# Performance work log

Measured on AMD Instinct MI355X. Metric: run time of the kernel, lower is better.

The kernel has to match this reference:

```python
import jax, jax.numpy as jnp
import numpy as np

NEG_SLOPE = 0.2


def gat_conv(x, src, dst, n, W, a_src, a_dst, b):
    # x: [N, Din], W: [Din, Dout], a_src/a_dst: [Dout], b: [Dout]
    h = x @ W                                   # [N, Dout]
    alpha_src = h @ a_src                       # [N] score contribution of source nodes
    alpha_dst = h @ a_dst                       # [N]
    e = jax.nn.leaky_relu(alpha_src[src] + alpha_dst[dst], NEG_SLOPE)  # [E]
    # segment softmax over destination nodes (every node has a self-loop -> no empty segs)
    m = jax.ops.segment_max(e, dst, num_segments=n)
    p = jnp.exp(e - m[dst])
    denom = jax.ops.segment_sum(p, dst, num_segments=n)
    coeff = p / denom[dst]                      # [E]
    out = jax.ops.segment_sum(h[src] * coeff[:, None], dst, num_segments=n)
    return out + b


def setup_inputs() -> dict:
    key = jax.random.key(0)
    ks = jax.random.split(key, 16)
    N, E, D_IN, D_H, C = 50000, 800000, 256, 256, 10
    x = jax.random.normal(ks[0], (N, D_IN), dtype=jnp.float32)
    edge_index = jax.random.randint(ks[1], (2, E), 0, N, dtype=jnp.int64)
    s = 0.1
    params = {
        "W1": jax.random.normal(ks[2], (D_IN, D_H), jnp.float32) * s,
        "a_src1": jax.random.normal(ks[3], (D_H,), jnp.float32) * s,
        "a_dst1": jax.random.normal(ks[4], (D_H,), jnp.float32) * s,
        "b1": jnp.zeros((D_H,), jnp.float32),
        "W2": jax.random.normal(ks[5], (D_H, D_H), jnp.float32) * s,
        "a_src2": jax.random.normal(ks[6], (D_H,), jnp.float32) * s,
        "a_dst2": jax.random.normal(ks[7], (D_H,), jnp.float32) * s,
        "b2": jnp.zeros((D_H,), jnp.float32),
        "W3": jax.random.normal(ks[8], (D_H, C), jnp.float32) * s,
        "a_src3": jax.random.normal(ks[9], (C,), jnp.float32) * s,
        "a_dst3": jax.random.normal(ks[10], (C,), jnp.float32) * s,
        "b3": jnp.zeros((C,), jnp.float32),
    }
    return {"x": x, "edge_index": edge_index, **params}


def reference(x, edge_index, W1, a_src1, a_dst1, b1, W2, a_src2, a_dst2, b2,
              W3, a_src3, a_dst3, b3):
    n = x.shape[0]
    # PyG GATConv default add_self_loops=True
    loops = jnp.arange(n, dtype=edge_index.dtype)
    src = jnp.concatenate([edge_index[0], loops])
    dst = jnp.concatenate([edge_index[1], loops])
    h = gat_conv(x, src, dst, n, W1, a_src1, a_dst1, b1)
    h = jax.nn.relu(h)
    h = gat_conv(h, src, dst, n, W2, a_src2, a_dst2, b2)
    h = jax.nn.relu(h)
    out = gat_conv(h, src, dst, n, W3, a_src3, a_dst3, b3)
    return out
```

## Files before the change

kernel.cpp:

```cpp
#include <hip/hip_runtime.h>
#include <math.h>

#define N_NODES 50000
#define N_EDGES 800000
#define EP (N_EDGES + N_NODES)
#define NEG_SLOPE 0.2f
#define SCAN_BLOCKS ((N_NODES + 255) / 256)
#define COUNT_BLOCKS ((EP + 255) / 256)

typedef short short8 __attribute__((ext_vector_type(8)));
typedef float float4_ __attribute__((ext_vector_type(4)));

__device__ __forceinline__ unsigned short f2bf(float f) {
  unsigned int u = __float_as_uint(f);
  u = (u + 0x7FFFu + ((u >> 16) & 1u)) >> 16;
  return (unsigned short)u;
}
__device__ __forceinline__ float bf2f(unsigned int us) {
  return __uint_as_float(us << 16);
}
__device__ __forceinline__ unsigned int pack2(float lo, float hi) {
  return (unsigned int)f2bf(lo) | ((unsigned int)f2bf(hi) << 16);
}

__device__ __forceinline__ int permc(int p) {
  return ((p & 0xE) << 4) | ((p & 1) << 4) | (p >> 4);
}


__global__ void setup_kernel(const float* __restrict__ W1, const float* __restrict__ W2,
                             const float* __restrict__ W3, const float* __restrict__ b1,
                             const float* __restrict__ b2, const int* __restrict__ ei,
                             unsigned short* __restrict__ Wf1, unsigned short* __restrict__ Wf2,
                             unsigned short* __restrict__ Wf3,
                             float* __restrict__ pb1, float* __restrict__ pb2,
                             int* __restrict__ cnt) {
  int blk = blockIdx.x;
  int tid = threadIdx.x;
  if (blk >= 67) {
    int e = (blk - 67) * 256 + tid;
    if (e < EP) {
      int dst = (e < N_EDGES) ? ei[N_EDGES + e] : (e - N_EDGES);
      atomicAdd(&cnt[dst], 1);
    }
    return;
  }
  if (blk < 64) {
    int perm = blk >= 32;
    const float* W = perm ? W2 : W1;
    unsigned short* Wf = perm ? Wf2 : Wf1;
    int t = (blk & 31) * 256 + tid;
    int f = t >> 6, lane = t & 63;
    int nt = f >> 3, k0t = f & 7;
    int lm = lane & 15, kg = lane >> 4;
    int kbase = k0t * 32 + kg * 8;
    int n = nt * 16 + lm;
    short8 v;
#pragma unroll
    for (int j = 0; j < 8; ++j) {
      int k = perm ? permc(kbase + j) : (kbase + j);
      v[j] = (short)f2bf(W[(size_t)k * 256 + n]);
    }
    ((short8*)Wf)[t] = v;
  } else if (blk < 66) {
    int t = (blk - 64) * 256 + tid;
    int k0t = t >> 6, lane = t & 63;
    int lm = lane & 15, kg = lane >> 4;
    int kbase = k0t * 32 + kg * 8;
    short8 v;
#pragma unroll
    for (int j = 0; j < 8; ++j) {
      int k = permc(kbase + j);
      v[j] = (lm < 10) ? (short)f2bf(W3[(size_t)k * 10 + lm]) : (short)0;
    }
    ((short8*)Wf3)[t] = v;
  } else {
    int c = permc(tid);
    pb1[tid] = b1[c];
    pb2[tid] = b2[c];
  }
}


__global__ void scan12_kernel(const int* __restrict__ cnt, int* __restrict__ off,
                              int* __restrict__ bsum, int* __restrict__ bpre,
                              int* __restrict__ done) {
  int i = blockIdx.x * 256 + threadIdx.x;
  int v = (i < N_NODES) ? cnt[i] : 0;
  int lane = threadIdx.x & 63, w = threadIdx.x >> 6;
  int x = v;
  for (int o = 1; o < 64; o <<= 1) { int y = __shfl_up(x, o); if (lane >= o) x += y; }
  __shared__ int wsum[4];
  if (lane == 63) wsum[w] = x;
  __syncthreads();
  int add = 0;
  for (int k = 0; k < w; ++k) add += wsum[k];
  if (i < N_NODES) off[i] = x - v + add;
  __shared__ int amLast;
  if (threadIdx.x == 255) {
    bsum[blockIdx.x] = add + x;
    __threadfence();
    amLast = (atomicAdd(done, 1) == SCAN_BLOCKS - 1);
  }
  __syncthreads();
  if (amLast) {
    int t = threadIdx.x;
    int v2 = (t < SCAN_BLOCKS) ? atomicAdd(&bsum[t], 0) : 0;
    int x2 = v2;
    for (int o = 1; o < 64; o <<= 1) { int y = __shfl_up(x2, o); if (lane >= o) x2 += y; }
    __shared__ int wsum2[4];
    if (lane == 63) wsum2[w] = x2;
    __syncthreads();
    int add2 = 0;
    for (int k = 0; k < w; ++k) add2 += wsum2[k];
    if (t < SCAN_BLOCKS) bpre[t] = x2 - v2 + add2;
    if (t == SCAN_BLOCKS - 1) off[N_NODES] = v2;
  }
}

__global__ void scatter_kernel(const int* __restrict__ ei, const int* __restrict__ off,
                               const int* __restrict__ bpre, int* __restrict__ cnt,
                               int* __restrict__ esrc) {
  int e = blockIdx.x * 256 + threadIdx.x;
  if (e >= EP) return;
  int src, dst;
  if (e < N_EDGES) { src = ei[e]; dst = ei[N_EDGES + e]; }
  else { src = dst = e - N_EDGES; }
  int pos = off[dst] + bpre[dst >> 8] + atomicSub(&cnt[dst], 1) - 1;
  esrc[pos] = src;
}


template <int AF32>
__global__ __launch_bounds__(896, 1) void gemm_mfma5(const void* __restrict__ Av,
                                                     const uint4* __restrict__ Wf,
                                                     unsigned short* __restrict__ C,
                                                     const float* __restrict__ asrc,
                                                     const float* __restrict__ adst,
                                                     float* __restrict__ as_,
                                                     float* __restrict__ ad_, int M) {
  __shared__ uint4 Bl[8192];
  int tid = threadIdx.x;
  for (int i = tid; i < 8192; i += 896) Bl[i] = Wf[i];
  int wave = tid >> 6, lane = tid & 63;
  int lm = lane & 15, kg = lane >> 4;
  int row0 = blockIdx.x * 224 + wave * 16;
  int ar = row0 + lm;
  if (ar >= M) ar = M - 1;
  float4_ acc[16];
#pragma unroll
  for (int i = 0; i < 16; ++i) acc[i] = (float4_){0, 0, 0, 0};
  __syncthreads();
  const short8* Bf = (const short8*)Bl;
  for (int k0t = 0; k0t < 8; ++k0t) {
    int k0 = k0t * 32;
    short8 a;
    if (AF32) {
      const float* A = (const float*)Av;
      const float* p = A + (size_t)ar * 256 + kg * 8 + k0;
      float4 f0 = *(const float4*)p, f1 = *(const float4*)(p + 4);
      a = (short8){(short)f2bf(f0.x), (short)f2bf(f0.y), (short)f2bf(f0.z), (short)f2bf(f0.w),
                   (short)f2bf(f1.x), (short)f2bf(f1.y), (short)f2bf(f1.z), (short)f2bf(f1.w)};
    } else {
      const unsigned short* A = (const unsigned short*)Av;
      a = *(const short8*)(A + (size_t)ar * 256 + kg * 8 + k0);
    }
#pragma unroll
    for (int nt = 0; nt < 16; ++nt) {
      short8 b = Bf[(nt * 8 + k0t) * 64 + lane];
      acc[nt] = __builtin_amdgcn_mfma_f32_16x16x32_bf16(a, b, acc[nt], 0, 0, 0);
    }
  }
  float avs[16], avd[16];
#pragma unroll
  for (int nt = 0; nt < 16; ++nt) { avs[nt] = asrc[nt * 16 + lm]; avd[nt] = adst[nt * 16 + lm]; }
#pragma unroll
  for (int i = 0; i < 4; ++i) {
    int r = row0 + kg * 4 + i;
    float s = 0.f, dd = 0.f;
    unsigned int u[8];
#pragma unroll
    for (int j = 0; j < 8; ++j) {
      float vlo = acc[2 * j][i];
      float vhi = acc[2 * j + 1][i];
      u[j] = pack2(vlo, vhi);
      s += vlo * avs[2 * j] + vhi * avs[2 * j + 1];
      dd += vlo * avd[2 * j] + vhi * avd[2 * j + 1];
    }
    if (r < M) {
      uint4* cp = (uint4*)(C + (size_t)r * 256 + lm * 16);
      cp[0] = (uint4){u[0], u[1], u[2], u[3]};
      cp[1] = (uint4){u[4], u[5], u[6], u[7]};
    }
#pragma unroll
    for (int o = 1; o < 16; o <<= 1) { s += __shfl_xor(s, o); dd += __shfl_xor(dd, o); }
    if (lm == 0 && r < M) { as_[r] = s; ad_[r] = dd; }
  }
}


__global__ __launch_bounds__(448) void gemm_c3_kernel(const unsigned short* __restrict__ X,
                                                      const unsigned short* __restrict__ Wf3,
                                                      const float* __restrict__ asrc,
                                                      const float* __restrict__ adst,
                                                      float* __restrict__ h3,
                                                      float* __restrict__ as_,
                                                      float* __restrict__ ad_, int M) {
  int tid = threadIdx.x;
  int wave = tid >> 6, lane = tid & 63;
  int lm = lane & 15, kg = lane >> 4;
  int row0 = blockIdx.x * 224 + wave * 32;
  int ar0 = row0 + lm, ar1 = row0 + 16 + lm;
  if (ar0 >= M) ar0 = M - 1;
  if (ar1 >= M) ar1 = M - 1;
  short8 bf[8];
#pragma unroll
  for (int k0t = 0; k0t < 8; ++k0t) bf[k0t] = ((const short8*)Wf3)[k0t * 64 + lane];
  float4_ acc0 = (float4_){0, 0, 0, 0}, acc1 = (float4_){0, 0, 0, 0};
#pragma unroll
  for (int k0t = 0; k0t < 8; ++k0t) {
    int k0 = k0t * 32;
    short8 a0 = *(const short8*)(X + (size_t)ar0 * 256 + kg * 8 + k0);
    short8 a1 = *(const short8*)(X + (size_t)ar1 * 256 + kg * 8 + k0);
    acc0 = __builtin_amdgcn_mfma_f32_16x16x32_bf16(a0, bf[k0t], acc0, 0, 0, 0);
    acc1 = __builtin_amdgcn_mfma_f32_16x16x32_bf16(a1, bf[k0t], acc1, 0, 0, 0);
  }
  float avs = (lm < 10) ? asrc[lm] : 0.f;
  float avd = (lm < 10) ? adst[lm] : 0.f;
#pragma unroll
  for (int g = 0; g < 2; ++g) {
    int rbase = row0 + g * 16 + kg * 4;
#pragma unroll
    for (int i = 0; i < 4; ++i) {
      int r = rbase + i;
      float v = g ? acc1[i] : acc0[i];
      if (r < M && lm < 10) h3[(size_t)r * 10 + lm] = v;
      float s = v * avs, dd = v * avd;
#pragma unroll
      for (int o = 1; o < 16; o <<= 1) { s += __shfl_xor(s, o); dd += __shfl_xor(dd, o); }
      if (lm == 0 && r < M) { as_[r] = s; ad_[r] = dd; }
    }
  }
}


__global__ __launch_bounds__(256) void agg_fused_kernel(const int* __restrict__ off,
                                                        const int* __restrict__ bpre,
                                                        const int* __restrict__ esrc,
                                                        const float* __restrict__ as_,
                                                        const float* __restrict__ ad_,
                                                        const unsigned short* __restrict__ h,
                                                        const float* __restrict__ pbias,
                                                        unsigned short* __restrict__ outg) {
  __shared__ int s_src[4][64];
  __shared__ float s_p[4][64];
  int wave = threadIdx.x >> 6, lane = threadIdx.x & 63;
  int pair = lane >> 5, cl = lane & 31;
  int d = blockIdx.x * 4 + wave;
  int s0 = off[d] + bpre[d >> 8];
  int s1 = off[d + 1] + bpre[(d + 1) >> 8];
  float adv = ad_[d];
  const uint4* hp4 = (const uint4*)h;
  float a0 = 0.f, a1 = 0.f, a2 = 0.f, a3 = 0.f, a4 = 0.f, a5 = 0.f, a6 = 0.f, a7 = 0.f;
  float sum = 0.f;
  for (int base = s0; base < s1; base += 64) {
    int m = s1 - base; if (m > 64) m = 64;
    int sv = 0; float p = 0.f;
    if (lane < m) {
      sv = esrc[base + lane];
      float e = as_[sv] + adv;
      e = e > 0.f ? e : NEG_SLOPE * e;
      p = __expf(e);
    }
    s_src[wave][lane] = sv;
    s_p[wave][lane] = p;
    float ps = p;
    for (int o = 32; o; o >>= 1) ps += __shfl_xor(ps, o);
    sum += ps;
    int nb = (m + 1) >> 1;
    int j = 0;
    for (; j + 4 <= nb; j += 4) {
#pragma unroll
      for (int u = 0; u < 4; ++u) {
        int idx = (j + u) * 2 + pair;
        int src = s_src[wave][idx];
        float w = s_p[wave][idx];
        uint4 pv = hp4[(size_t)src * 32 + cl];
        a0 = fmaf(w, bf2f(pv.x & 0xffffu), a0); a1 = fmaf(w, bf2f(pv.x >> 16), a1);
        a2 = fmaf(w, bf2f(pv.y & 0xffffu), a2); a3 = fmaf(w, bf2f(pv.y >> 16), a3);
        a4 = fmaf(w, bf2f(pv.z & 0xffffu), a4); a5 = fmaf(w, bf2f(pv.z >> 16), a5);
        a6 = fmaf(w, bf2f(pv.w & 0xffffu), a6); a7 = fmaf(w, bf2f(pv.w >> 16), a7);
      }
    }
    for (; j < nb; ++j) {
      int idx = j * 2 + pair;
      int src = s_src[wave][idx];
      float w = s_p[wave][idx];
      uint4 pv = hp4[(size_t)src * 32 + cl];
      a0 = fmaf(w, bf2f(pv.x & 0xffffu), a0); a1 = fmaf(w, bf2f(pv.x >> 16), a1);
      a2 = fmaf(w, bf2f(pv.y & 0xffffu), a2); a3 = fmaf(w, bf2f(pv.y >> 16), a3);
      a4 = fmaf(w, bf2f(pv.z & 0xffffu), a4); a5 = fmaf(w, bf2f(pv.z >> 16), a5);
      a6 = fmaf(w, bf2f(pv.w & 0xffffu), a6); a7 = fmaf(w, bf2f(pv.w >> 16), a7);
    }
  }
  a0 += __shfl_xor(a0, 32); a1 += __shfl_xor(a1, 32);
  a2 += __shfl_xor(a2, 32); a3 += __shfl_xor(a3, 32);
  a4 += __shfl_xor(a4, 32); a5 += __shfl_xor(a5, 32);
  a6 += __shfl_xor(a6, 32); a7 += __shfl_xor(a7, 32);
  if (pair == 0) {
    float inv = 1.0f / sum;
    float4 b0 = ((const float4*)pbias)[2 * cl];
    float4 b1 = ((const float4*)pbias)[2 * cl + 1];
    float o0 = fmaxf(fmaf(a0, inv, b0.x), 0.f);
    float o1 = fmaxf(fmaf(a1, inv, b0.y), 0.f);
    float o2 = fmaxf(fmaf(a2, inv, b0.z), 0.f);
    float o3 = fmaxf(fmaf(a3, inv, b0.w), 0.f);
    float o4 = fmaxf(fmaf(a4, inv, b1.x), 0.f);
    float o5 = fmaxf(fmaf(a5, inv, b1.y), 0.f);
    float o6 = fmaxf(fmaf(a6, inv, b1.z), 0.f);
    float o7 = fmaxf(fmaf(a7, inv, b1.w), 0.f);
    uint4 ov = (uint4){pack2(o0, o1), pack2(o2, o3), pack2(o4, o5), pack2(o6, o7)};
    ((uint4*)outg)[(size_t)d * 32 + cl] = ov;
  }
}


__global__ void agg10_fused_kernel(const int* __restrict__ off, const int* __restrict__ bpre,
                                   const int* __restrict__ esrc,
                                   const float* __restrict__ as_, const float* __restrict__ ad_,
                                   const float* __restrict__ h, const float* __restrict__ bias,
                                   float* __restrict__ out) {
  int gid = blockIdx.x * 256 + threadIdx.x;
  int wid = gid >> 6, lane = threadIdx.x & 63;
  int g = lane >> 4, c = lane & 15;
  int d = wid * 4 + g;
  if (d >= N_NODES) return;
  int s0 = off[d] + bpre[d >> 8];
  int s1 = off[d + 1] + bpre[(d + 1) >> 8];
  float adv = ad_[d];
  float acc = 0.f, sum = 0.f;
  int s = s0;
  for (; s + 2 <= s1; s += 2) {
    int i0 = esrc[s], i1 = esrc[s + 1];
    float e0 = as_[i0] + adv; e0 = e0 > 0.f ? e0 : NEG_SLOPE * e0;
    float e1 = as_[i1] + adv; e1 = e1 > 0.f ? e1 : NEG_SLOPE * e1;
    float h0 = (c < 10) ? h[(size_t)i0 * 10 + c] : 0.f;
    float h1 = (c < 10) ? h[(size_t)i1 * 10 + c] : 0.f;
    float p0 = __expf(e0), p1 = __expf(e1);
    acc = fmaf(p0, h0, acc);
    acc = fmaf(p1, h1, acc);
    sum += p0 + p1;
  }
  if (s < s1) {
    int i0 = esrc[s];
    float e0 = as_[i0] + adv; e0 = e0 > 0.f ? e0 : NEG_SLOPE * e0;
    float p0 = __expf(e0);
    if (c < 10) acc = fmaf(p0, h[(size_t)i0 * 10 + c], acc);
    sum += p0;
  }
  if (c < 10) out[(size_t)d * 10 + c] = fmaf(acc, 1.0f / sum, bias[c]);
}


extern "C" void kernel_launch(void* const* d_in, const int* in_sizes, int n_in,
                              void* d_out, int out_size, void* d_ws, size_t ws_size,
                              hipStream_t stream) {
  const float* x   = (const float*)d_in[0];
  const int*   ei  = (const int*)d_in[1];
  const float* W1  = (const float*)d_in[2];
  const float* as1 = (const float*)d_in[3];
  const float* ad1 = (const float*)d_in[4];
  const float* b1  = (const float*)d_in[5];
  const float* W2  = (const float*)d_in[6];
  const float* as2 = (const float*)d_in[7];
  const float* ad2 = (const float*)d_in[8];
  const float* b2  = (const float*)d_in[9];
  const float* W3  = (const float*)d_in[10];
  const float* as3 = (const float*)d_in[11];
  const float* ad3 = (const float*)d_in[12];
  const float* b3  = (const float*)d_in[13];
  float* out = (float*)d_out;

  char* ws = (char*)d_ws;
  size_t off_b = 0;
  auto alloc = [&](size_t bytes) -> char* {
    char* p = ws + off_b;
    off_b += (bytes + 255) & ~(size_t)255;
    return p;
  };
  unsigned short* hb   = (unsigned short*)alloc((size_t)N_NODES * 256 * 2);
  unsigned short* gb   = (unsigned short*)alloc((size_t)N_NODES * 256 * 2);
  unsigned short* Wf1  = (unsigned short*)alloc(256 * 256 * 2);
  unsigned short* Wf2  = (unsigned short*)alloc(256 * 256 * 2);
  unsigned short* Wf3  = (unsigned short*)alloc(8 * 64 * 8 * 2);
  float* pb1   = (float*)alloc(256 * 4);
  float* pb2   = (float*)alloc(256 * 4);
  float* h3    = (float*)alloc((size_t)N_NODES * 10 * 4);
  float* as_   = (float*)alloc((size_t)N_NODES * 4);
  float* ad_   = (float*)alloc((size_t)N_NODES * 4);
  int*   roff  = (int*)alloc((size_t)(N_NODES + 1) * 4);
  int*   cnt   = (int*)alloc((size_t)(N_NODES + 64) * 4);
  int*   done  = cnt + N_NODES;
  int*   bsum  = (int*)alloc((size_t)SCAN_BLOCKS * 4);
  int*   bpre  = (int*)alloc((size_t)SCAN_BLOCKS * 4);
  int*   esrc  = (int*)alloc((size_t)EP * 4);

  hipMemsetAsync(cnt, 0, (size_t)(N_NODES + 1) * 4, stream);
  setup_kernel<<<67 + COUNT_BLOCKS, 256, 0, stream>>>(W1, W2, W3, b1, b2, ei,
                                                      Wf1, Wf2, Wf3, pb1, pb2, cnt);
  scan12_kernel<<<SCAN_BLOCKS, 256, 0, stream>>>(cnt, roff, bsum, bpre, done);
  scatter_kernel<<<COUNT_BLOCKS, 256, 0, stream>>>(ei, roff, bpre, cnt, esrc);

  int gblocks = (N_NODES + 223) / 224;
  int ablocks = (N_NODES + 3) / 4;

  gemm_mfma5<1><<<gblocks, 896, 0, stream>>>(x, (const uint4*)Wf1, hb, as1, ad1, as_, ad_, N_NODES);
  agg_fused_kernel<<<ablocks, 256, 0, stream>>>(roff, bpre, esrc, as_, ad_, hb, pb1, gb);
  gemm_mfma5<0><<<gblocks, 896, 0, stream>>>(gb, (const uint4*)Wf2, hb, as2, ad2, as_, ad_, N_NODES);
  agg_fused_kernel<<<ablocks, 256, 0, stream>>>(roff, bpre, esrc, as_, ad_, hb, pb2, gb);
  gemm_c3_kernel<<<gblocks, 448, 0, stream>>>(gb, Wf3, as3, ad3, h3, as_, ad_, N_NODES);
  agg10_fused_kernel<<<ablocks, 256, 0, stream>>>(roff, bpre, esrc, as_, ad_, h3, b3, out);
}
```

Before: 371.5 us.

## Fuse layer-3 projection into layer-2 aggregation epilogue and widen GEMM blocks

Removes the separate layer-3 GEMM kernel by computing the 10-wide projection and the folded attention scores (W3·a_src3, W3·a_dst3 precomputed in setup) in the epilogue of the second aggregation, using fp32 weights held in shared memory and a 32-lane shuffle reduction. This avoids rereading the 50000x256 bf16 activation buffer and saves a kernel launch. It also enlarges the GEMM blocks from 896 to 1024 threads (256 rows each) and adds an occupancy hint of 8 blocks for the aggregation kernel. In exchange the second aggregation carries extra shared memory, extra FMAs and a shuffle reduction per node, which may lower its occupancy.

```diff
diff --git a/kernel.cpp b/kernel.cpp
--- a/kernel.cpp
+++ b/kernel.cpp
@@ -30,15 +30,15 @@
 
 __global__ void setup_kernel(const float* __restrict__ W1, const float* __restrict__ W2,
                              const float* __restrict__ W3, const float* __restrict__ b1,
-                             const float* __restrict__ b2, const int* __restrict__ ei,
+                             const float* __restrict__ b2, const float* __restrict__ as3,
+                             const float* __restrict__ ad3, const int* __restrict__ ei,
                              unsigned short* __restrict__ Wf1, unsigned short* __restrict__ Wf2,
-                             unsigned short* __restrict__ Wf3,
                              float* __restrict__ pb1, float* __restrict__ pb2,
-                             int* __restrict__ cnt) {
+                             float* __restrict__ W3p, int* __restrict__ cnt) {
   int blk = blockIdx.x;
   int tid = threadIdx.x;
-  if (blk >= 67) {
-    int e = (blk - 67) * 256 + tid;
+  if (blk >= 65) {
+    int e = (blk - 65) * 256 + tid;
     if (e < EP) {
       int dst = (e < N_EDGES) ? ei[N_EDGES + e] : (e - N_EDGES);
       atomicAdd(&cnt[dst], 1);
@@ -62,22 +62,22 @@
       v[j] = (short)f2bf(W[(size_t)k * 256 + n]);
     }
     ((short8*)Wf)[t] = v;
-  } else if (blk < 66) {
-    int t = (blk - 64) * 256 + tid;
-    int k0t = t >> 6, lane = t & 63;
-    int lm = lane & 15, kg = lane >> 4;
-    int kbase = k0t * 32 + kg * 8;
-    short8 v;
-#pragma unroll
-    for (int j = 0; j < 8; ++j) {
-      int k = permc(kbase + j);
-      v[j] = (lm < 10) ? (short)f2bf(W3[(size_t)k * 10 + lm]) : (short)0;
-    }
-    ((short8*)Wf3)[t] = v;
   } else {
     int c = permc(tid);
     pb1[tid] = b1[c];
     pb2[tid] = b2[c];
+    const float* wr = W3 + (size_t)c * 10;
+    float s = 0.f, dd = 0.f;
+#pragma unroll
+    for (int j = 0; j < 10; ++j) {
+      float w = wr[j];
+      W3p[tid * 13 + j] = w;
+      s += w * as3[j];
+      dd += w * ad3[j];
+    }
+    W3p[tid * 13 + 10] = s;
+    W3p[tid * 13 + 11] = dd;
+    W3p[tid * 13 + 12] = 0.f;
   }
 }
 
@@ -132,19 +132,19 @@
 
 
 template <int AF32>
-__global__ __launch_bounds__(896, 1) void gemm_mfma5(const void* __restrict__ Av,
-                                                     const uint4* __restrict__ Wf,
-                                                     unsigned short* __restrict__ C,
-                                                     const float* __restrict__ asrc,
-                                                     const float* __restrict__ adst,
-                                                     float* __restrict__ as_,
-                                                     float* __restrict__ ad_, int M) {
+__global__ __launch_bounds__(1024, 1) void gemm_mfma5(const void* __restrict__ Av,
+                                                      const uint4* __restrict__ Wf,
+                                                      unsigned short* __restrict__ C,
+                                                      const float* __restrict__ asrc,
+                                                      const float* __restrict__ adst,
+                                                      float* __restrict__ as_,
+                                                      float* __restrict__ ad_, int M) {
   __shared__ uint4 Bl[8192];
   int tid = threadIdx.x;
-  for (int i = tid; i < 8192; i += 896) Bl[i] = Wf[i];
+  for (int i = tid; i < 8192; i += 1024) Bl[i] = Wf[i];
   int wave = tid >> 6, lane = tid & 63;
   int lm = lane & 15, kg = lane >> 4;
-  int row0 = blockIdx.x * 224 + wave * 16;
+  int row0 = blockIdx.x * 256 + wave * 16;
   int ar = row0 + lm;
   if (ar >= M) ar = M - 1;
   float4_ acc[16];
@@ -199,61 +199,26 @@
 }
 
 
-__global__ __launch_bounds__(448) void gemm_c3_kernel(const unsigned short* __restrict__ X,
-                                                      const unsigned short* __restrict__ Wf3,
-                                                      const float* __restrict__ asrc,
-                                                      const float* __restrict__ adst,
-                                                      float* __restrict__ h3,
-                                                      float* __restrict__ as_,
-                                                      float* __restrict__ ad_, int M) {
-  int tid = threadIdx.x;
-  int wave = tid >> 6, lane = tid & 63;
-  int lm = lane & 15, kg = lane >> 4;
-  int row0 = blockIdx.x * 224 + wave * 32;
-  int ar0 = row0 + lm, ar1 = row0 + 16 + lm;
-  if (ar0 >= M) ar0 = M - 1;
-  if (ar1 >= M) ar1 = M - 1;
-  short8 bf[8];
-#pragma unroll
-  for (int k0t = 0; k0t < 8; ++k0t) bf[k0t] = ((const short8*)Wf3)[k0t * 64 + lane];
-  float4_ acc0 = (float4_){0, 0, 0, 0}, acc1 = (float4_){0, 0, 0, 0};
-#pragma unroll
-  for (int k0t = 0; k0t < 8; ++k0t) {
-    int k0 = k0t * 32;
-    short8 a0 = *(const short8*)(X + (size_t)ar0 * 256 + kg * 8 + k0);
-    short8 a1 = *(const short8*)(X + (size_t)ar1 * 256 + kg * 8 + k0);
-    acc0 = __builtin_amdgcn_mfma_f32_16x16x32_bf16(a0, bf[k0t], acc0, 0, 0, 0);
-    acc1 = __builtin_amdgcn_mfma_f32_16x16x32_bf16(a1, bf[k0t], acc1, 0, 0, 0);
-  }
-  float avs = (lm < 10) ? asrc[lm] : 0.f;
-  float avd = (lm < 10) ? adst[lm] : 0.f;
-#pragma unroll
-  for (int g = 0; g < 2; ++g) {
-    int rbase = row0 + g * 16 + kg * 4;
-#pragma unroll
-    for (int i = 0; i < 4; ++i) {
-      int r = rbase + i;
-      float v = g ? acc1[i] : acc0[i];
-      if (r < M && lm < 10) h3[(size_t)r * 10 + lm] = v;
-      float s = v * avs, dd = v * avd;
-#pragma unroll
-      for (int o = 1; o < 16; o <<= 1) { s += __shfl_xor(s, o); dd += __shfl_xor(dd, o); }
-      if (lm == 0 && r < M) { as_[r] = s; ad_[r] = dd; }
-    }
-  }
-}
-
-
-__global__ __launch_bounds__(256) void agg_fused_kernel(const int* __restrict__ off,
-                                                        const int* __restrict__ bpre,
-                                                        const int* __restrict__ esrc,
-                                                        const float* __restrict__ as_,
-                                                        const float* __restrict__ ad_,
-                                                        const unsigned short* __restrict__ h,
-                                                        const float* __restrict__ pbias,
-                                                        unsigned short* __restrict__ outg) {
+template <int W3EP>
+__global__ __launch_bounds__(256, 8) void agg_fused_kernel(const int* __restrict__ off,
+                                                           const int* __restrict__ bpre,
+                                                           const int* __restrict__ esrc,
+                                                           const float* __restrict__ as_,
+                                                           const float* __restrict__ ad_,
+                                                           const unsigned short* __restrict__ h,
+                                                           const float* __restrict__ pbias,
+                                                           unsigned short* __restrict__ outg,
+                                                           const float* __restrict__ W3p,
+                                                           float* __restrict__ h3,
+                                                           float* __restrict__ as3b,
+                                                           float* __restrict__ ad3b) {
   __shared__ int s_src[4][64];
   __shared__ float s_p[4][64];
+  __shared__ float sW3p[W3EP ? 3328 : 1];
+  if (W3EP) {
+    for (int i = threadIdx.x; i < 3328; i += 256) sW3p[i] = W3p[i];
+    __syncthreads();
+  }
   int wave = threadIdx.x >> 6, lane = threadIdx.x & 63;
   int pair = lane >> 5, cl = lane & 31;
   int d = blockIdx.x * 4 + wave;
@@ -311,16 +276,41 @@
     float inv = 1.0f / sum;
     float4 b0 = ((const float4*)pbias)[2 * cl];
     float4 b1 = ((const float4*)pbias)[2 * cl + 1];
-    float o0 = fmaxf(fmaf(a0, inv, b0.x), 0.f);
-    float o1 = fmaxf(fmaf(a1, inv, b0.y), 0.f);
-    float o2 = fmaxf(fmaf(a2, inv, b0.z), 0.f);
-    float o3 = fmaxf(fmaf(a3, inv, b0.w), 0.f);
-    float o4 = fmaxf(fmaf(a4, inv, b1.x), 0.f);
-    float o5 = fmaxf(fmaf(a5, inv, b1.y), 0.f);
-    float o6 = fmaxf(fmaf(a6, inv, b1.z), 0.f);
-    float o7 = fmaxf(fmaf(a7, inv, b1.w), 0.f);
-    uint4 ov = (uint4){pack2(o0, o1), pack2(o2, o3), pack2(o4, o5), pack2(o6, o7)};
+    float o[8];
+    o[0] = fmaxf(fmaf(a0, inv, b0.x), 0.f);
+    o[1] = fmaxf(fmaf(a1, inv, b0.y), 0.f);
+    o[2] = fmaxf(fmaf(a2, inv, b0.z), 0.f);
+    o[3] = fmaxf(fmaf(a3, inv, b0.w), 0.f);
+    o[4] = fmaxf(fmaf(a4, inv, b1.x), 0.f);
+    o[5] = fmaxf(fmaf(a5, inv, b1.y), 0.f);
+    o[6] = fmaxf(fmaf(a6, inv, b1.z), 0.f);
+    o[7] = fmaxf(fmaf(a7, inv, b1.w), 0.f);
+    uint4 ov = (uint4){pack2(o[0], o[1]), pack2(o[2], o[3]), pack2(o[4], o[5]), pack2(o[6], o[7])};
     ((uint4*)outg)[(size_t)d * 32 + cl] = ov;
+    if (W3EP) {
+      float pr[12];
+#pragma unroll
+      for (int c = 0; c < 12; ++c) pr[c] = 0.f;
+#pragma unroll
+      for (int j = 0; j < 8; ++j) {
+        float ovl = o[j];
+        const float* wr = &sW3p[(cl * 8 + j) * 13];
+#pragma unroll
+        for (int c = 0; c < 12; ++c) pr[c] = fmaf(ovl, wr[c], pr[c]);
+      }
+#pragma unroll
+      for (int ofs = 1; ofs < 32; ofs <<= 1) {
+#pragma unroll
+        for (int c = 0; c < 12; ++c) pr[c] += __shfl_xor(pr[c], ofs);
+      }
+      if (cl == 0) {
+        float* hp = h3 + (size_t)d * 10;
+#pragma unroll
+        for (int c = 0; c < 10; ++c) hp[c] = pr[c];
+        as3b[d] = pr[10];
+        ad3b[d] = pr[11];
+      }
+    }
   }
 }
 
@@ -392,12 +382,14 @@
   unsigned short* gb   = (unsigned short*)alloc((size_t)N_NODES * 256 * 2);
   unsigned short* Wf1  = (unsigned short*)alloc(256 * 256 * 2);
   unsigned short* Wf2  = (unsigned short*)alloc(256 * 256 * 2);
-  unsigned short* Wf3  = (unsigned short*)alloc(8 * 64 * 8 * 2);
+  float* W3p   = (float*)alloc(3328 * 4);
   float* pb1   = (float*)alloc(256 * 4);
   float* pb2   = (float*)alloc(256 * 4);
   float* h3    = (float*)alloc((size_t)N_NODES * 10 * 4);
   float* as_   = (float*)alloc((size_t)N_NODES * 4);
   float* ad_   = (float*)alloc((size_t)N_NODES * 4);
+  float* as3b  = (float*)alloc((size_t)N_NODES * 4);
+  float* ad3b  = (float*)alloc((size_t)N_NODES * 4);
   int*   roff  = (int*)alloc((size_t)(N_NODES + 1) * 4);
   int*   cnt   = (int*)alloc((size_t)(N_NODES + 64) * 4);
   int*   done  = cnt + N_NODES;
@@ -406,18 +398,19 @@
   int*   esrc  = (int*)alloc((size_t)EP * 4);
 
   hipMemsetAsync(cnt, 0, (size_t)(N_NODES + 1) * 4, stream);
-  setup_kernel<<<67 + COUNT_BLOCKS, 256, 0, stream>>>(W1, W2, W3, b1, b2, ei,
-                                                      Wf1, Wf2, Wf3, pb1, pb2, cnt);
+  setup_kernel<<<65 + COUNT_BLOCKS, 256, 0, stream>>>(W1, W2, W3, b1, b2, as3, ad3, ei,
+                                                      Wf1, Wf2, pb1, pb2, W3p, cnt);
   scan12_kernel<<<SCAN_BLOCKS, 256, 0, stream>>>(cnt, roff, bsum, bpre, done);
   scatter_kernel<<<COUNT_BLOCKS, 256, 0, stream>>>(ei, roff, bpre, cnt, esrc);
 
-  int gblocks = (N_NODES + 223) / 224;
+  int gblocks = (N_NODES + 255) / 256;
   int ablocks = (N_NODES + 3) / 4;
 
-  gemm_mfma5<1><<<gblocks, 896, 0, stream>>>(x, (const uint4*)Wf1, hb, as1, ad1, as_, ad_, N_NODES);
-  agg_fused_kernel<<<ablocks, 256, 0, stream>>>(roff, bpre, esrc, as_, ad_, hb, pb1, gb);
-  gemm_mfma5<0><<<gblocks, 896, 0, stream>>>(gb, (const uint4*)Wf2, hb, as2, ad2, as_, ad_, N_NODES);
-  agg_fused_kernel<<<ablocks, 256, 0, stream>>>(roff, bpre, esrc, as_, ad_, hb, pb2, gb);
-  gemm_c3_kernel<<<gblocks, 448, 0, stream>>>(gb, Wf3, as3, ad3, h3, as_, ad_, N_NODES);
-  agg10_fused_kernel<<<ablocks, 256, 0, stream>>>(roff, bpre, esrc, as_, ad_, h3, b3, out);
-}
+  gemm_mfma5<1><<<gblocks, 1024, 0, stream>>>(x, (const uint4*)Wf1, hb, as1, ad1, as_, ad_, N_NODES);
+  agg_fused_kernel<0><<<ablocks, 256, 0, stream>>>(roff, bpre, esrc, as_, ad_, hb, pb1, gb,
+                                                   nullptr, nullptr, nullptr, nullptr);
+  gemm_mfma5<0><<<gblocks, 1024, 0, stream>>>(gb, (const uint4*)Wf2, hb, as2, ad2, as_, ad_, N_NODES);
+  agg_fused_kernel<1><<<ablocks, 256, 0, stream>>>(roff, bpre, esrc, as_, ad_, hb, pb2, gb,
+                                                   W3p, h3, as3b, ad3b);
+  agg10_fused_kernel<<<ablocks, 256, 0, stream>>>(roff, bpre, esrc, as3b, ad3b, h3, b3, out);
+}
```

Result: slower. 432.8 us (+16.5%).
